# Performance work log

Measured on AMD Instinct MI355X. Metric: run time of the kernel, lower is better.

Reference implementation:

```python
import jax, jax.numpy as jnp
import numpy as np
import math

B, S, DIM = 2, 2048, 2048
H, HD, RD = 16, 128, 64
LKV, LQ = 512, 1536

def _rope(x, cos, sin):
    # x: (B,S,H,RD); interpret consecutive pairs as complex, multiply by e^{i theta}
    b, s, h, d = x.shape
    xr = x.reshape(b, s, h, d // 2, 2)
    xre, xim = xr[..., 0], xr[..., 1]
    c = cos[None, :, None, :]  # (1,S,1,d/2)
    sn = sin[None, :, None, :]
    ore = xre * c - xim * sn
    oim = xre * sn + xim * c
    return jnp.stack([ore, oim], axis=-1).reshape(b, s, h, d)

def setup_inputs() -> dict:
    key = jax.random.key(0)
    ks = jax.random.split(key, 12)
    def w(k, shape, fan_in):
        return jax.random.normal(k, shape, jnp.float32) * (1.0 / math.sqrt(fan_in))
    x = jax.random.normal(ks[0], (B, S, DIM), jnp.float32)
    # RoPE tables for decoupled rotary subspace of width RD
    inv_freq = 1.0 / (10000.0 ** (np.arange(0, RD, 2, dtype=np.float32) / RD))
    ang = np.outer(np.arange(S, dtype=np.float32), inv_freq)  # (S, RD/2)
    freq_cos = jnp.asarray(np.cos(ang), jnp.float32)
    freq_sin = jnp.asarray(np.sin(ang), jnp.float32)
    return {
        "x": x, "freq_cos": freq_cos, "freq_sin": freq_sin,
        "Wkv": w(ks[1], (DIM, LKV), DIM),          # latent_kv (no bias)
        "Wlq": w(ks[2], (DIM, LQ), DIM),           # latent_q (no bias)
        "Wq": w(ks[3], (LQ, H * HD), LQ),          # query (no bias)
        "Wk": w(ks[4], (LKV, H * HD), LKV),        # key (no bias)
        "Wv": w(ks[5], (LKV, H * HD), LKV),        # value (no bias)
        "Wqr": w(ks[6], (LQ, H * RD), LQ),         # decop_rot_q (bias=True)
        "bqr": jnp.zeros((H * RD,), jnp.float32),
        "Wkr": w(ks[7], (DIM, H * RD), DIM),       # decop_rot_k (bias=True)
        "bkr": jnp.zeros((H * RD,), jnp.float32),
        "Wo": w(ks[8], (H * HD, DIM), H * HD),     # out_proj (bias=True)
        "bo": jnp.zeros((DIM,), jnp.float32),
    }

def reference(x, freq_cos, freq_sin, Wkv, Wlq, Wq, Wk, Wv, Wqr, bqr, Wkr, bkr, Wo, bo):
    b, s, _ = x.shape
    cq = x @ Wlq                      # (B,S,LQ)
    ckv = x @ Wkv                     # (B,S,LKV)
    q = (cq @ Wq).reshape(b, s, H, HD)
    qr = _rope((cq @ Wqr + bqr).reshape(b, s, H, RD), freq_cos, freq_sin)
    k = (ckv @ Wk).reshape(b, s, H, HD)
    kr = _rope((x @ Wkr + bkr).reshape(b, s, H, RD), freq_cos, freq_sin)
    v = (ckv @ Wv).reshape(b, s, H, HD)
    qf = jnp.concatenate([q, qr], axis=-1)   # (B,S,H,HD+RD)
    kf = jnp.concatenate([k, kr], axis=-1)
    scale = 1.0 / math.sqrt(HD + RD)
    scores = jnp.einsum('bqhd,bkhd->bhqk', qf, kf) * scale
    # masked=True path: causal tril mask over full seq_len
    mask = jnp.tril(jnp.ones((s, s), bool))
    scores = jnp.where(mask[None, None], scores, -jnp.inf)
    att = jax.nn.softmax(scores.astype(jnp.float32), axis=-1).astype(qf.dtype)
    out = jnp.einsum('bhqk,bkhd->bqhd', att, v).reshape(b, s, H * HD)
    return out @ Wo + bo
```

## Files before the change

### kernel.cpp

```cpp
#include <hip/hip_runtime.h>
#include <hip/hip_bf16.h>
#include <stdint.h>

#define S_LEN 2048
#define NB 2
#define NH 16
#define HDIM 128
#define RDIM 64
#define DF 192
#define MROWS 4096

typedef __bf16 bf16_t;
typedef __attribute__((ext_vector_type(8))) __bf16 bf16x8;
typedef __attribute__((ext_vector_type(4))) __bf16 bf16x4;
typedef __attribute__((ext_vector_type(4))) float f32x4;
typedef __attribute__((ext_vector_type(4))) float float4v;

__device__ __forceinline__ void gload_lds16(const bf16_t* g, bf16_t* l) {
  __builtin_amdgcn_global_load_lds(
      (const __attribute__((address_space(1))) void*)g,
      (__attribute__((address_space(3))) void*)l, 16, 0, 0);
}

__global__ __launch_bounds__(256) void convert_bf16(const float* __restrict__ in,
                                                    bf16_t* __restrict__ out, int n4) {
  int i = blockIdx.x * 256 + threadIdx.x;
  if (i >= n4) return;
  float4v v = *reinterpret_cast<const float4v*>(&in[(size_t)i * 4]);
  bf16x4 o;
  o[0] = (bf16_t)v[0]; o[1] = (bf16_t)v[1]; o[2] = (bf16_t)v[2]; o[3] = (bf16_t)v[3];
  *reinterpret_cast<bf16x4*>(&out[(size_t)i * 4]) = o;
}

struct TrDesc { const float* src; bf16_t* dst; int K; int N; int nbx; int base; };
struct TrPack { TrDesc d[8]; };

__global__ __launch_bounds__(256) void transpose_all(TrPack p) {
  __shared__ float t[64][65];
  const int bid = blockIdx.x;
  int m = 0;
#pragma unroll
  for (int i = 1; i < 8; ++i) m += (bid >= p.d[i].base);
  const TrDesc td = p.d[m];
  const int local = bid - td.base;
  const int n0 = (local % td.nbx) * 64, k0 = (local / td.nbx) * 64;
  const int tx = threadIdx.x & 63, ty = threadIdx.x >> 6;
#pragma unroll
  for (int i = ty; i < 64; i += 4)
    t[i][tx] = td.src[(size_t)(k0 + i) * td.N + n0 + tx];
  __syncthreads();
#pragma unroll
  for (int i = ty; i < 64; i += 4)
    td.dst[(size_t)(n0 + i) * td.K + k0 + tx] = (bf16_t)t[tx][i];
}

struct EpiParams {
  bf16_t* o0;
  bf16_t* o1;
  bf16_t* o2;
  float* outf;
  const float* bias;
  const float* cosb;
  const float* sinb;
};

template <int MODE>
__device__ __forceinline__ void gemm8p_body(const bf16_t* __restrict__ A,
                                            const bf16_t* __restrict__ Bt,
                                            int N, int K, int m0, int n0,
                                            bf16_t (*Ab)[256 * 64],
                                            bf16_t (*Bb)[128 * 64], EpiParams ep) {
  const int tid = threadIdx.x;
  const int lane = tid & 63, w = tid >> 6;
  const int l15 = lane & 15, lg = lane >> 4;
  const int mw = (w >> 1) * 64, nw = (w & 1) * 64;
  const int nt = K >> 6;

  auto stage = [&](int t, int buf) {
    const int k0 = t << 6;
#pragma unroll
    for (int j = 0; j < 4; ++j) {
      const int s = j * 512 + tid;
      const int row = s >> 3, c = s & 7;
      const int cs = c ^ (row & 7);
      gload_lds16(A + (size_t)(m0 + row) * K + k0 + cs * 8, &Ab[buf][s * 8]);
    }
#pragma unroll
    for (int j = 0; j < 2; ++j) {
      const int s = j * 512 + tid;
      const int row = s >> 3, c = s & 7;
      const int cs = c ^ (row & 7);
      gload_lds16(Bt + (size_t)(n0 + row) * K + k0 + cs * 8, &Bb[buf][s * 8]);
    }
  };

  f32x4 acc[4][4] = {};
  stage(0, 0);
  stage(1, 1);

  for (int t = 0; t < nt; ++t) {
    const int cur = t % 3;
    if (t + 1 < nt) {
      asm volatile("s_waitcnt vmcnt(6)" ::: "memory");
    } else {
      asm volatile("s_waitcnt vmcnt(0)" ::: "memory");
    }
    __builtin_amdgcn_s_barrier();
    __builtin_amdgcn_sched_barrier(0);
    if (t + 2 < nt) stage(t + 2, (t + 2) % 3);

    __builtin_amdgcn_s_setprio(1);
#pragma unroll
    for (int kk = 0; kk < 2; ++kk) {
      const int c = kk * 4 + lg;
      bf16x8 a[4], b[4];
#pragma unroll
      for (int i = 0; i < 4; ++i) {
        const int r = mw + i * 16 + l15;
        a[i] = *reinterpret_cast<const bf16x8*>(&Ab[cur][r * 64 + ((c ^ (r & 7)) << 3)]);
      }
#pragma unroll
      for (int j = 0; j < 4; ++j) {
        const int r = nw + j * 16 + l15;
        b[j] = *reinterpret_cast<const bf16x8*>(&Bb[cur][r * 64 + ((c ^ (r & 7)) << 3)]);
      }
#pragma unroll
      for (int i = 0; i < 4; ++i)
#pragma unroll
        for (int j = 0; j < 4; ++j)
          acc[i][j] = __builtin_amdgcn_mfma_f32_16x16x32_bf16(a[i], b[j], acc[i][j], 0, 0, 0);
    }
    __builtin_amdgcn_s_setprio(0);
  }

#pragma unroll
  for (int i = 0; i < 4; ++i)
#pragma unroll
    for (int j = 0; j < 4; ++j) {
      const int col = n0 + nw + j * 16 + l15;
#pragma unroll
      for (int r = 0; r < 4; ++r) {
        const int row = m0 + mw + i * 16 + lg * 4 + r;
        float v = acc[i][j][r];
        const int b = row >> 11, s = row & 2047;
        if constexpr (MODE == 1) {
          ep.outf[(size_t)row * N + col] = v + ep.bias[col];
        } else if constexpr (MODE == 5) {
          if (col < 1536) {
            ep.o0[(size_t)row * 1536 + col] = (bf16_t)v;
          } else if (col < 2048) {
            ep.o1[(size_t)row * 512 + (col - 1536)] = (bf16_t)v;
          } else {
            const int c2 = col - 2048;
            float vb = v + ep.bias[c2];
            float other = __shfl_xor(vb, 1, 64);
            const int h = c2 >> 6, dr = c2 & 63;
            const int fi = dr >> 1;
            const float c = ep.cosb[s * 32 + fi];
            const float sn = ep.sinb[s * 32 + fi];
            const float o = (c2 & 1) ? (other * sn + vb * c) : (vb * c - other * sn);
            ep.o2[(((size_t)(b * NH + h)) * S_LEN + s) * DF + 128 + dr] = (bf16_t)o;
          }
        } else if constexpr (MODE == 6) {
          if (col < 2048) {
            const int h = col >> 7, d = col & 127;
            ep.o0[(((size_t)(b * NH + h)) * S_LEN + s) * DF + d] = (bf16_t)v;
          } else {
            const int c2 = col - 2048;
            float vb = v + ep.bias[c2];
            float other = __shfl_xor(vb, 1, 64);
            const int h = c2 >> 6, dr = c2 & 63;
            const int fi = dr >> 1;
            const float c = ep.cosb[s * 32 + fi];
            const float sn = ep.sinb[s * 32 + fi];
            const float o = (c2 & 1) ? (other * sn + vb * c) : (vb * c - other * sn);
            ep.o0[(((size_t)(b * NH + h)) * S_LEN + s) * DF + 128 + dr] = (bf16_t)o;
          }
        } else {
          if (col < 2048) {
            const int h = col >> 7, d = col & 127;
            ep.o0[(((size_t)(b * NH + h)) * S_LEN + s) * DF + d] = (bf16_t)v;
          } else {
            const int c2 = col - 2048;
            const int h = c2 >> 7, d = c2 & 127;
            ep.o1[(((size_t)(b * NH + h)) * HDIM + d) * S_LEN + s] = (bf16_t)v;
          }
        }
      }
    }
}

template <int MODE>
__global__ __launch_bounds__(512, 2) void gemm8p(const bf16_t* __restrict__ A,
                                                 const bf16_t* __restrict__ Bt,
                                                 int N, int K, EpiParams ep) {
  __shared__ alignas(16) bf16_t Ab[3][256 * 64];
  __shared__ alignas(16) bf16_t Bb[3][128 * 64];
  const int nwg = gridDim.x;
  int f = blockIdx.x;
  f = (f & 7) * (nwg >> 3) + (f >> 3);
  const int nbx = N >> 7;
  const int m0 = (f / nbx) * 256, n0 = (f % nbx) * 128;
  gemm8p_body<MODE>(A, Bt, N, K, m0, n0, Ab, Bb, ep);
}

__global__ __launch_bounds__(512, 2) void gemm8p67(const bf16_t* __restrict__ A6,
                                                   const bf16_t* __restrict__ Bt6,
                                                   const bf16_t* __restrict__ A7,
                                                   const bf16_t* __restrict__ Bt7,
                                                   EpiParams ep6, EpiParams ep7) {
  __shared__ alignas(16) bf16_t Ab[3][256 * 64];
  __shared__ alignas(16) bf16_t Bb[3][128 * 64];
  const int bid = blockIdx.x;
  if (bid < 384) {
    int f = (bid & 7) * 48 + (bid >> 3);
    const int m0 = (f / 24) * 256, n0 = (f % 24) * 128;
    gemm8p_body<6>(A6, Bt6, 3072, 1536, m0, n0, Ab, Bb, ep6);
  } else {
    int b2 = bid - 384;
    int f = (b2 & 7) * 64 + (b2 >> 3);
    const int m0 = (f / 32) * 256, n0 = (f % 32) * 128;
    gemm8p_body<7>(A7, Bt7, 4096, 512, m0, n0, Ab, Bb, ep7);
  }
}

__global__ __launch_bounds__(256, 2) void attn_fwd(const bf16_t* __restrict__ qf,
                                                   const bf16_t* __restrict__ kf,
                                                   const bf16_t* __restrict__ vT,
                                                   bf16_t* __restrict__ att) {
  const int tid = threadIdx.x;
  const int lane = tid & 63, w = tid >> 6;
  const int l15 = lane & 15, lg = lane >> 4;
  const int l = blockIdx.x;
  const int bh = (l & 7) * 4 + ((l >> 3) & 3);
  const int qchunk = l >> 5;
  const int qb0 = (15 - qchunk) * 128;
  const int q0 = qb0 + w * 32;
  const float scale = 0.07216878364870322f;

  __shared__ alignas(16) bf16_t Ks[64 * 192];
  __shared__ alignas(16) bf16_t Vs[128 * 64];
  __shared__ alignas(16) bf16_t Ps[4 * 2048];

  bf16x8 qfr[2][6];
#pragma unroll
  for (int mf = 0; mf < 2; ++mf) {
    const bf16_t* qptr = qf + ((size_t)bh * S_LEN + q0 + mf * 16 + l15) * DF + lg * 8;
#pragma unroll
    for (int d = 0; d < 6; ++d)
      qfr[mf][d] = *reinterpret_cast<const bf16x8*>(qptr + d * 32);
  }

  f32x4 o[2][8] = {};
  float mrun[2] = {-1e30f, -1e30f}, lsum[2] = {0.0f, 0.0f};

  const bf16_t* kb0 = kf + (size_t)bh * S_LEN * DF;
  const bf16_t* vb0 = vT + (size_t)bh * HDIM * S_LEN;
  const int njt = qb0 / 64 + 2;
  const int wslot = tid & ~63;

  for (int jt = 0; jt < njt; ++jt) {
    const int j0 = jt * 64;
    __syncthreads();
    const bf16_t* kTile = kb0 + (size_t)j0 * DF;
#pragma unroll
    for (int i = 0; i < 6; ++i) {
      const int s = i * 256 + tid;
      const int row = s / 24;
      const int c = s - row * 24;
      const int cs = c ^ (row & 7);
      gload_lds16(kTile + (size_t)row * DF + cs * 8,
                  Ks + (size_t)(i * 256 + wslot) * 8);
    }
    const bf16_t* vTile = vb0 + j0;
#pragma unroll
    for (int i = 0; i < 4; ++i) {
      const int s = i * 256 + tid;
      const int row = s >> 3;
      const int c = s & 7;
      const int cs = c ^ (row & 7);
      gload_lds16(vTile + (size_t)row * S_LEN + cs * 8,
                  Vs + (size_t)(i * 256 + wslot) * 8);
    }
    __syncthreads();

    if (j0 > q0 + 31) continue;

    f32x4 sa[2][4] = {};
    __builtin_amdgcn_s_setprio(1);
#pragma unroll
    for (int jf = 0; jf < 4; ++jf) {
      const int krow = jf * 16 + l15;
      const int ksw = krow & 7;
#pragma unroll
      for (int d = 0; d < 6; ++d) {
        const int kc = (4 * d + lg) ^ ksw;
        bf16x8 kfr = *reinterpret_cast<const bf16x8*>(&Ks[krow * 192 + kc * 8]);
#pragma unroll
        for (int mf = 0; mf < 2; ++mf)
          sa[mf][jf] =
              __builtin_amdgcn_mfma_f32_16x16x32_bf16(kfr, qfr[mf][d], sa[mf][jf], 0, 0, 0);
      }
    }
    __builtin_amdgcn_s_setprio(0);

#pragma unroll
    for (int mf = 0; mf < 2; ++mf) {
      const int qi = q0 + mf * 16 + l15;
      const bool full = (j0 + 63 <= q0 + mf * 16);
      float sv[16];
#pragma unroll
      for (int jf = 0; jf < 4; ++jf)
#pragma unroll
        for (int r = 0; r < 4; ++r) {
          float x = sa[mf][jf][r] * scale;
          if (!full) {
            const int j = j0 + jf * 16 + lg * 4 + r;
            if (j > qi) x = -1e30f;
          }
          sv[jf * 4 + r] = x;
        }

      float a8[8];
#pragma unroll
      for (int i = 0; i < 8; ++i) a8[i] = fmaxf(sv[i], sv[i + 8]);
#pragma unroll
      for (int i = 0; i < 4; ++i) a8[i] = fmaxf(a8[i], a8[i + 4]);
      float mx = fmaxf(fmaxf(a8[0], a8[1]), fmaxf(a8[2], a8[3]));
      mx = fmaxf(mx, __shfl_xor(mx, 16, 64));
      mx = fmaxf(mx, __shfl_xor(mx, 32, 64));

      if (__any(mx > mrun[mf] + 8.0f)) {
        const float mn = fmaxf(mrun[mf], mx);
        const float alpha = __expf(mrun[mf] - mn);
        mrun[mf] = mn;
        lsum[mf] *= alpha;
        float af[4];
#pragma unroll
        for (int r = 0; r < 4; ++r) af[r] = __shfl(alpha, lg * 4 + r, 16);
#pragma unroll
        for (int dt = 0; dt < 8; ++dt)
#pragma unroll
          for (int r = 0; r < 4; ++r) o[mf][dt][r] *= af[r];
      }

#pragma unroll
      for (int i = 0; i < 16; ++i) sv[i] = __expf(sv[i] - mrun[mf]);
      float s8[8];
#pragma unroll
      for (int i = 0; i < 8; ++i) s8[i] = sv[i] + sv[i + 8];
#pragma unroll
      for (int i = 0; i < 4; ++i) s8[i] = s8[i] + s8[i + 4];
      float sm = (s8[0] + s8[1]) + (s8[2] + s8[3]);
      sm += __shfl_xor(sm, 16, 64);
      sm += __shfl_xor(sm, 32, 64);
      lsum[mf] += sm;

#pragma unroll
      for (int jf = 0; jf < 4; ++jf) {
        bf16x4 pk;
#pragma unroll
        for (int r = 0; r < 4; ++r) pk[r] = (bf16_t)sv[jf * 4 + r];
        const int key = jf * 16 + lg * 4;
        *reinterpret_cast<bf16x4*>(
            &Ps[w * 2048 + mf * 1024 + l15 * 64 + (key ^ ((l15 & 7) << 3))]) = pk;
      }
    }
    asm volatile("s_waitcnt lgkmcnt(0)" ::: "memory");
    __builtin_amdgcn_sched_barrier(0);
    bf16x8 pfr[2][2];
#pragma unroll
    for (int mf = 0; mf < 2; ++mf)
#pragma unroll
      for (int jk = 0; jk < 2; ++jk)
        pfr[mf][jk] = *reinterpret_cast<const bf16x8*>(
            &Ps[w * 2048 + mf * 1024 + l15 * 64 + (((jk * 4 + lg) ^ (l15 & 7)) << 3)]);

    __builtin_amdgcn_s_setprio(1);
#pragma unroll
    for (int dt = 0; dt < 8; ++dt) {
      const int vrow = dt * 16 + l15;
      const int vsw = vrow & 7;
#pragma unroll
      for (int jk = 0; jk < 2; ++jk) {
        const int vc = (jk * 4 + lg) ^ vsw;
        bf16x8 vfr = *reinterpret_cast<const bf16x8*>(&Vs[vrow * 64 + vc * 8]);
#pragma unroll
        for (int mf = 0; mf < 2; ++mf)
          o[mf][dt] =
              __builtin_amdgcn_mfma_f32_16x16x32_bf16(pfr[mf][jk], vfr, o[mf][dt], 0, 0, 0);
      }
    }
    __builtin_amdgcn_s_setprio(0);
  }

  const int b = bh >> 4, h = bh & 15;
#pragma unroll
  for (int mf = 0; mf < 2; ++mf) {
    const float inv = 1.0f / lsum[mf];
    float iv[4];
#pragma unroll
    for (int r = 0; r < 4; ++r) iv[r] = __shfl(inv, lg * 4 + r, 16);
#pragma unroll
    for (int dt = 0; dt < 8; ++dt)
#pragma unroll
      for (int r = 0; r < 4; ++r) {
        const int s = q0 + mf * 16 + lg * 4 + r;
        att[((size_t)b * S_LEN + s) * 2048 + h * 128 + dt * 16 + l15] =
            (bf16_t)(o[mf][dt][r] * iv[r]);
      }
  }
}

extern "C" void kernel_launch(void* const* d_in, const int* in_sizes, int n_in,
                              void* d_out, int out_size, void* d_ws, size_t ws_size,
                              hipStream_t stream) {
  const float* x    = (const float*)d_in[0];
  const float* fcos = (const float*)d_in[1];
  const float* fsin = (const float*)d_in[2];
  const float* Wkv  = (const float*)d_in[3];
  const float* Wlq  = (const float*)d_in[4];
  const float* Wq   = (const float*)d_in[5];
  const float* Wk   = (const float*)d_in[6];
  const float* Wv   = (const float*)d_in[7];
  const float* Wqr  = (const float*)d_in[8];
  const float* bqr  = (const float*)d_in[9];
  const float* Wkr  = (const float*)d_in[10];
  const float* bkr  = (const float*)d_in[11];
  const float* Wo   = (const float*)d_in[12];
  const float* bo   = (const float*)d_in[13];
  float* out = (float*)d_out;

  char* ws = (char*)d_ws;
  size_t off = 0;
  auto alloc = [&](size_t bytes) {
    void* p = ws + off;
    off += (bytes + 255) & ~(size_t)255;
    return p;
  };
  bf16_t* xb    = (bf16_t*)alloc((size_t)MROWS * 2048 * 2);
  bf16_t* WcatA = (bf16_t*)alloc((size_t)3072 * 2048 * 2);
  bf16_t* WcatB = (bf16_t*)alloc((size_t)3072 * 1536 * 2);
  bf16_t* WcatC = (bf16_t*)alloc((size_t)4096 * 512 * 2);
  bf16_t* WoT   = (bf16_t*)alloc((size_t)2048 * 2048 * 2);
  bf16_t* cq    = (bf16_t*)alloc((size_t)MROWS * 1536 * 2);
  bf16_t* ckv   = (bf16_t*)alloc((size_t)MROWS * 512 * 2);
  bf16_t* qfb   = (bf16_t*)alloc((size_t)NB * NH * S_LEN * DF * 2);
  bf16_t* kfb   = (bf16_t*)alloc((size_t)NB * NH * S_LEN * DF * 2);
  bf16_t* vTb   = (bf16_t*)alloc((size_t)NB * NH * HDIM * S_LEN * 2);
  bf16_t* attb  = (bf16_t*)alloc((size_t)MROWS * 2048 * 2);

  {
    int n4 = (MROWS * 2048) / 4;
    convert_bf16<<<dim3((n4 + 255) / 256), dim3(256), 0, stream>>>(x, xb, n4);
  }
  {
    TrPack p;
    int base = 0;
    auto set = [&](int i, const float* s, bf16_t* d, int K, int N) {
      p.d[i] = {s, d, K, N, N / 64, base};
      base += (N / 64) * (K / 64);
    };
    set(0, Wlq, WcatA, 2048, 1536);
    set(1, Wkv, WcatA + (size_t)1536 * 2048, 2048, 512);
    set(2, Wkr, WcatA + (size_t)2048 * 2048, 2048, 1024);
    set(3, Wq,  WcatB, 1536, 2048);
    set(4, Wqr, WcatB + (size_t)2048 * 1536, 1536, 1024);
    set(5, Wk,  WcatC, 512, 2048);
    set(6, Wv,  WcatC + (size_t)2048 * 512, 512, 2048);
    set(7, Wo,  WoT, 2048, 2048);
    transpose_all<<<dim3(base), dim3(256), 0, stream>>>(p);
  }

  EpiParams ep{}, ep2{};

  ep = {cq, ckv, kfb, nullptr, bkr, fcos, fsin};
  gemm8p<5><<<dim3(384), dim3(512), 0, stream>>>(xb, WcatA, 3072, 2048, ep);
  ep  = {qfb, nullptr, nullptr, nullptr, bqr, fcos, fsin};
  ep2 = {kfb, vTb, nullptr, nullptr, nullptr, nullptr, nullptr};
  gemm8p67<<<dim3(896), dim3(512), 0, stream>>>(cq, WcatB, ckv, WcatC, ep, ep2);
  attn_fwd<<<dim3(512), dim3(256), 0, stream>>>(qfb, kfb, vTb, attb);
  ep = {nullptr, nullptr, nullptr, out, bo, nullptr, nullptr};
  gemm8p<1><<<dim3(256), dim3(512), 0, stream>>>(attb, WoT, 2048, 2048, ep);
}
```

Measured before the change: 382.2 us.

## Replace triple-buffered GEMM pipeline with double-buffered four-phase interleaved schedule

Reworks the shared GEMM mainloop from a three-stage LDS ring with prefetch distance two to a two-buffer scheme. Each k-tile is split into four phases that interleave LDS fragment reads, next-tile global-to-LDS loads and half-width MFMA groups, separated by barriers. The aim is finer-grained overlap of memory and matrix work and a smaller LDS footprint. In exchange it adds many more workgroup barriers per tile and shortens the prefetch lead time, which could expose load latency.

```diff
diff --git a/kernel.cpp b/kernel.cpp
--- a/kernel.cpp
+++ b/kernel.cpp
@@ -65,72 +65,89 @@
 };
 
 template <int MODE>
-__device__ __forceinline__ void gemm8p_body(const bf16_t* __restrict__ A,
-                                            const bf16_t* __restrict__ Bt,
-                                            int N, int K, int m0, int n0,
-                                            bf16_t (*Ab)[256 * 64],
-                                            bf16_t (*Bb)[128 * 64], EpiParams ep) {
+__device__ __forceinline__ void gemm_body(const bf16_t* __restrict__ A,
+                                          const bf16_t* __restrict__ Bt,
+                                          int N, int K, int m0, int n0,
+                                          bf16_t (*Ab)[256 * 64],
+                                          bf16_t (*Bb)[128 * 64], EpiParams ep) {
   const int tid = threadIdx.x;
   const int lane = tid & 63, w = tid >> 6;
   const int l15 = lane & 15, lg = lane >> 4;
   const int mw = (w >> 1) * 64, nw = (w & 1) * 64;
   const int nt = K >> 6;
 
-  auto stage = [&](int t, int buf) {
-    const int k0 = t << 6;
-#pragma unroll
-    for (int j = 0; j < 4; ++j) {
-      const int s = j * 512 + tid;
-      const int row = s >> 3, c = s & 7;
-      const int cs = c ^ (row & 7);
-      gload_lds16(A + (size_t)(m0 + row) * K + k0 + cs * 8, &Ab[buf][s * 8]);
-    }
-#pragma unroll
-    for (int j = 0; j < 2; ++j) {
-      const int s = j * 512 + tid;
-      const int row = s >> 3, c = s & 7;
-      const int cs = c ^ (row & 7);
-      gload_lds16(Bt + (size_t)(n0 + row) * K + k0 + cs * 8, &Bb[buf][s * 8]);
-    }
+  auto stageA = [&](int t, int buf, int j) {
+    const int s = j * 512 + tid;
+    const int row = s >> 3, c = s & 7;
+    const int cs = c ^ (row & 7);
+    gload_lds16(A + (size_t)(m0 + row) * K + (t << 6) + cs * 8, &Ab[buf][s * 8]);
   };
+  auto stageB = [&](int t, int buf, int j) {
+    const int s = j * 512 + tid;
+    const int row = s >> 3, c = s & 7;
+    const int cs = c ^ (row & 7);
+    gload_lds16(Bt + (size_t)(n0 + row) * K + (t << 6) + cs * 8, &Bb[buf][s * 8]);
+  };
 
   f32x4 acc[4][4] = {};
-  stage(0, 0);
-  stage(1, 1);
+#pragma unroll
+  for (int j = 0; j < 4; ++j) stageA(0, 0, j);
+#pragma unroll
+  for (int j = 0; j < 2; ++j) stageB(0, 0, j);
+  asm volatile("s_waitcnt vmcnt(0)" ::: "memory");
+  __builtin_amdgcn_s_barrier();
 
   for (int t = 0; t < nt; ++t) {
-    const int cur = t % 3;
-    if (t + 1 < nt) {
-      asm volatile("s_waitcnt vmcnt(6)" ::: "memory");
-    } else {
-      asm volatile("s_waitcnt vmcnt(0)" ::: "memory");
-    }
-    __builtin_amdgcn_s_barrier();
-    __builtin_amdgcn_sched_barrier(0);
-    if (t + 2 < nt) stage(t + 2, (t + 2) % 3);
-
-    __builtin_amdgcn_s_setprio(1);
-#pragma unroll
-    for (int kk = 0; kk < 2; ++kk) {
+    const int cur = t & 1;
+    const bool pf = (t + 1 < nt);
+    bf16x8 a[4], b[4];
+#pragma unroll
+    for (int p = 0; p < 4; ++p) {
+      const int kk = p >> 1, ih = p & 1;
       const int c = kk * 4 + lg;
-      bf16x8 a[4], b[4];
-#pragma unroll
-      for (int i = 0; i < 4; ++i) {
-        const int r = mw + i * 16 + l15;
-        a[i] = *reinterpret_cast<const bf16x8*>(&Ab[cur][r * 64 + ((c ^ (r & 7)) << 3)]);
-      }
-#pragma unroll
-      for (int j = 0; j < 4; ++j) {
-        const int r = nw + j * 16 + l15;
-        b[j] = *reinterpret_cast<const bf16x8*>(&Bb[cur][r * 64 + ((c ^ (r & 7)) << 3)]);
-      }
-#pragma unroll
-      for (int i = 0; i < 4; ++i)
-#pragma unroll
-        for (int j = 0; j < 4; ++j)
-          acc[i][j] = __builtin_amdgcn_mfma_f32_16x16x32_bf16(a[i], b[j], acc[i][j], 0, 0, 0);
-    }
-    __builtin_amdgcn_s_setprio(0);
+      if (ih == 0) {
+#pragma unroll
+        for (int i = 0; i < 4; ++i) {
+          const int r = mw + i * 16 + l15;
+          a[i] = *reinterpret_cast<const bf16x8*>(&Ab[cur][r * 64 + ((c ^ (r & 7)) << 3)]);
+        }
+#pragma unroll
+        for (int j = 0; j < 2; ++j) {
+          const int r = nw + j * 16 + l15;
+          b[j] = *reinterpret_cast<const bf16x8*>(&Bb[cur][r * 64 + ((c ^ (r & 7)) << 3)]);
+        }
+      } else {
+#pragma unroll
+        for (int j = 2; j < 4; ++j) {
+          const int r = nw + j * 16 + l15;
+          b[j] = *reinterpret_cast<const bf16x8*>(&Bb[cur][r * 64 + ((c ^ (r & 7)) << 3)]);
+        }
+      }
+      if (pf) {
+        if (p == 0) { stageA(t + 1, cur ^ 1, 0); stageA(t + 1, cur ^ 1, 1); stageA(t + 1, cur ^ 1, 2); }
+        if (p == 1) { stageA(t + 1, cur ^ 1, 3); stageB(t + 1, cur ^ 1, 0); stageB(t + 1, cur ^ 1, 1); }
+        if (p == 3) asm volatile("s_waitcnt vmcnt(0)" ::: "memory");
+      }
+      __builtin_amdgcn_s_barrier();
+      asm volatile("s_waitcnt lgkmcnt(0)" ::: "memory");
+      __builtin_amdgcn_sched_barrier(0);
+      __builtin_amdgcn_s_setprio(1);
+      if (ih == 0) {
+#pragma unroll
+        for (int i = 0; i < 4; ++i)
+#pragma unroll
+          for (int j = 0; j < 2; ++j)
+            acc[i][j] = __builtin_amdgcn_mfma_f32_16x16x32_bf16(a[i], b[j], acc[i][j], 0, 0, 0);
+      } else {
+#pragma unroll
+        for (int i = 0; i < 4; ++i)
+#pragma unroll
+          for (int j = 2; j < 4; ++j)
+            acc[i][j] = __builtin_amdgcn_mfma_f32_16x16x32_bf16(a[i], b[j], acc[i][j], 0, 0, 0);
+      }
+      __builtin_amdgcn_s_setprio(0);
+      __builtin_amdgcn_s_barrier();
+    }
   }
 
 #pragma unroll
@@ -191,36 +208,36 @@
 }
 
 template <int MODE>
-__global__ __launch_bounds__(512, 2) void gemm8p(const bf16_t* __restrict__ A,
-                                                 const bf16_t* __restrict__ Bt,
-                                                 int N, int K, EpiParams ep) {
-  __shared__ alignas(16) bf16_t Ab[3][256 * 64];
-  __shared__ alignas(16) bf16_t Bb[3][128 * 64];
+__global__ __launch_bounds__(512, 2) void gemm_4p(const bf16_t* __restrict__ A,
+                                                  const bf16_t* __restrict__ Bt,
+                                                  int N, int K, EpiParams ep) {
+  __shared__ alignas(16) bf16_t Ab[2][256 * 64];
+  __shared__ alignas(16) bf16_t Bb[2][128 * 64];
   const int nwg = gridDim.x;
   int f = blockIdx.x;
   f = (f & 7) * (nwg >> 3) + (f >> 3);
   const int nbx = N >> 7;
   const int m0 = (f / nbx) * 256, n0 = (f % nbx) * 128;
-  gemm8p_body<MODE>(A, Bt, N, K, m0, n0, Ab, Bb, ep);
-}
-
-__global__ __launch_bounds__(512, 2) void gemm8p67(const bf16_t* __restrict__ A6,
-                                                   const bf16_t* __restrict__ Bt6,
-                                                   const bf16_t* __restrict__ A7,
-                                                   const bf16_t* __restrict__ Bt7,
-                                                   EpiParams ep6, EpiParams ep7) {
-  __shared__ alignas(16) bf16_t Ab[3][256 * 64];
-  __shared__ alignas(16) bf16_t Bb[3][128 * 64];
+  gemm_body<MODE>(A, Bt, N, K, m0, n0, Ab, Bb, ep);
+}
+
+__global__ __launch_bounds__(512, 2) void gemm_4p67(const bf16_t* __restrict__ A6,
+                                                    const bf16_t* __restrict__ Bt6,
+                                                    const bf16_t* __restrict__ A7,
+                                                    const bf16_t* __restrict__ Bt7,
+                                                    EpiParams ep6, EpiParams ep7) {
+  __shared__ alignas(16) bf16_t Ab[2][256 * 64];
+  __shared__ alignas(16) bf16_t Bb[2][128 * 64];
   const int bid = blockIdx.x;
   if (bid < 384) {
     int f = (bid & 7) * 48 + (bid >> 3);
     const int m0 = (f / 24) * 256, n0 = (f % 24) * 128;
-    gemm8p_body<6>(A6, Bt6, 3072, 1536, m0, n0, Ab, Bb, ep6);
+    gemm_body<6>(A6, Bt6, 3072, 1536, m0, n0, Ab, Bb, ep6);
   } else {
     int b2 = bid - 384;
     int f = (b2 & 7) * 64 + (b2 >> 3);
     const int m0 = (f / 32) * 256, n0 = (f % 32) * 128;
-    gemm8p_body<7>(A7, Bt7, 4096, 512, m0, n0, Ab, Bb, ep7);
+    gemm_body<7>(A7, Bt7, 4096, 512, m0, n0, Ab, Bb, ep7);
   }
 }
 
@@ -475,11 +492,11 @@
   EpiParams ep{}, ep2{};
 
   ep = {cq, ckv, kfb, nullptr, bkr, fcos, fsin};
-  gemm8p<5><<<dim3(384), dim3(512), 0, stream>>>(xb, WcatA, 3072, 2048, ep);
+  gemm_4p<5><<<dim3(384), dim3(512), 0, stream>>>(xb, WcatA, 3072, 2048, ep);
   ep  = {qfb, nullptr, nullptr, nullptr, bqr, fcos, fsin};
   ep2 = {kfb, vTb, nullptr, nullptr, nullptr, nullptr, nullptr};
-  gemm8p67<<<dim3(896), dim3(512), 0, stream>>>(cq, WcatB, ckv, WcatC, ep, ep2);
+  gemm_4p67<<<dim3(896), dim3(512), 0, stream>>>(cq, WcatB, ckv, WcatC, ep, ep2);
   attn_fwd<<<dim3(512), dim3(256), 0, stream>>>(qfb, kfb, vTb, attb);
   ep = {nullptr, nullptr, nullptr, out, bo, nullptr, nullptr};
-  gemm8p<1><<<dim3(256), dim3(512), 0, stream>>>(attb, WoT, 2048, 2048, ep);
-}
+  gemm_4p<1><<<dim3(256), dim3(512), 0, stream>>>(attb, WoT, 2048, 2048, ep);
+}
```

Result: no change. 375.5 us (-1.8%).
